# Kernel optimization log

Hardware: AMD Instinct MI355X
Metric: run time of the kernel (lower is better)

The kernel has to match this reference:

```python
import jax, jax.numpy as jnp
import numpy as np

D_MODEL = 1024
NUM_HEADS = 16
D_K = D_MODEL // NUM_HEADS
NEG_INF = -1e9


def setup_inputs() -> dict:
    key = jax.random.key(0)
    ks = jax.random.split(key, 12)
    B, S = 2, 2048
    scale = 1.0 / np.sqrt(D_MODEL)
    inp = {
        "q": jax.random.normal(ks[0], (B, S, D_MODEL), jnp.float32),
        "k": jax.random.normal(ks[1], (B, S, D_MODEL), jnp.float32),
        "v": jax.random.normal(ks[2], (B, S, D_MODEL), jnp.float32),
        "mask": jnp.ones((B, S), jnp.int32),
        "W_q": jax.random.normal(ks[3], (D_MODEL, D_MODEL), jnp.float32) * scale,
        "b_q": jnp.zeros((D_MODEL,), jnp.float32),
        "W_k": jax.random.normal(ks[4], (D_MODEL, D_MODEL), jnp.float32) * scale,
        "b_k": jnp.zeros((D_MODEL,), jnp.float32),
        "W_v": jax.random.normal(ks[5], (D_MODEL, D_MODEL), jnp.float32) * scale,
        "b_v": jnp.zeros((D_MODEL,), jnp.float32),
        "W_o": jax.random.normal(ks[6], (D_MODEL, D_MODEL), jnp.float32) * scale,
        "b_o": jnp.zeros((D_MODEL,), jnp.float32),
    }
    return inp


def reference(q, k, v, mask, W_q, b_q, W_k, b_k, W_v, b_v, W_o, b_o):
    B, S, _ = q.shape
    def proj(x, W, b):
        # [B,S,D] -> [B,H,S,d_k]
        y = x @ W.T + b
        return y.reshape(B, -1, NUM_HEADS, D_K).transpose(0, 2, 1, 3)
    qh = proj(q, W_q, b_q)
    kh = proj(k, W_k, b_k)
    vh = proj(v, W_v, b_v)
    scores = jnp.einsum("bhqd,bhkd->bhqk", qh, kh) / jnp.sqrt(jnp.float32(D_K))
    # 2D mask [B,S_k] -> broadcast over heads and query positions
    m = mask[:, None, None, :]
    scores = jnp.where(m == 0, jnp.float32(NEG_INF), scores)
    attn = jax.nn.softmax(scores, axis=-1)
    # dropout is identity at inference
    context = jnp.einsum("bhqk,bhkd->bhqd", attn, vh)
    context = context.transpose(0, 2, 1, 3).reshape(B, S, D_MODEL)
    return context @ W_o.T + b_o
```

## Files before the change

### kernel.cpp

```cpp
#include <hip/hip_runtime.h>
#include <hip/hip_bf16.h>
#include <cstdint>
#include <cstddef>

#define DMODEL 1024
#define NHEADS 16
#define DK 64
#define SEQ 2048
#define BATCH 2
#define NT (SEQ / 32)

typedef short bf16x8 __attribute__((ext_vector_type(8)));
typedef float f32x4 __attribute__((ext_vector_type(4)));
typedef float f32x16 __attribute__((ext_vector_type(16)));
typedef unsigned int u32x2 __attribute__((ext_vector_type(2)));
typedef unsigned int u32x4 __attribute__((ext_vector_type(4)));

typedef const __attribute__((address_space(1))) void* gas_ptr;
typedef __attribute__((address_space(3))) void* las_ptr;

__device__ __forceinline__ void gld_lds16(const void* g, void* l) {
    __builtin_amdgcn_global_load_lds((gas_ptr)g, (las_ptr)l, 16, 0, 0);
}

__device__ __forceinline__ ushort f2bf_u(float f) {
    uint32_t x = __float_as_uint(f);
    x += 0x7fff + ((x >> 16) & 1);
    return (ushort)(x >> 16);
}

__global__ __launch_bounds__(256) void cast_all(
        const float* __restrict__ q, const float* __restrict__ k,
        const float* __restrict__ v, const float* __restrict__ Wq,
        const float* __restrict__ Wk, const float* __restrict__ Wv,
        const float* __restrict__ Wo,
        ushort* __restrict__ qb, ushort* __restrict__ kb, ushort* __restrict__ vb,
        ushort* __restrict__ Wqb, ushort* __restrict__ Wkb,
        ushort* __restrict__ Wvb, ushort* __restrict__ Wob) {
    int bid = blockIdx.x;
    const float* src; ushort* dst; int base;
    if      (bid <  4096) { src = q;  dst = qb;  base = bid; }
    else if (bid <  8192) { src = k;  dst = kb;  base = bid - 4096; }
    else if (bid < 12288) { src = v;  dst = vb;  base = bid - 8192; }
    else if (bid < 13312) { src = Wq; dst = Wqb; base = bid - 12288; }
    else if (bid < 14336) { src = Wk; dst = Wkb; base = bid - 13312; }
    else if (bid < 15360) { src = Wv; dst = Wvb; base = bid - 14336; }
    else                  { src = Wo; dst = Wob; base = bid - 15360; }
    int i = base * 1024 + threadIdx.x * 4;
    float4 f = *reinterpret_cast<const float4*>(src + i);
    ushort4 o;
    o.x = f2bf_u(f.x); o.y = f2bf_u(f.y); o.z = f2bf_u(f.z); o.w = f2bf_u(f.w);
    *reinterpret_cast<ushort4*>(dst + i) = o;
}

__global__ __launch_bounds__(256) void mask2bias(
        const int* __restrict__ m, float* __restrict__ mb) {
    int i = (blockIdx.x * 256 + threadIdx.x) * 4;
    int4 mk = *reinterpret_cast<const int4*>(m + i);
    float4 o;
    o.x = mk.x ? 0.f : -1e9f;
    o.y = mk.y ? 0.f : -1e9f;
    o.z = mk.z ? 0.f : -1e9f;
    o.w = mk.w ? 0.f : -1e9f;
    *reinterpret_cast<float4*>(mb + i) = o;
}

template<int MODE>
__global__ __launch_bounds__(256) void gemm_bt(
        const ushort* __restrict__ A,
        const ushort* __restrict__ W,
        const float* __restrict__ bias,
        void* __restrict__ out, int M, int N, int K) {
    __shared__ ushort As[64 * 32];
    __shared__ ushort Bs[128 * 32];
    const int tid = threadIdx.x;
    const int w = tid >> 6, lane = tid & 63;
    const int lr = lane & 15, lg = lane >> 4;
    const int nTiles = N >> 7;
    const int nwg = gridDim.x;
    const int cpx = nwg >> 3;
    int lid = (blockIdx.x & 7) * cpx + (blockIdx.x >> 3);
    const int tM = (lid / nTiles) << 6;
    const int tN = (lid % nTiles) << 7;
    const int wr = (w >> 1) * 32, wc = (w & 1) * 64;

    f32x4 acc[2][4] = {};

    const int cA = w * 64 + lane;
    const int cB0 = w * 128 + lane;
    const int cB1 = w * 128 + 64 + lane;
    const ushort* gA  = A + (size_t)(tM + (cA  >> 2)) * K + (cA  & 3) * 8;
    const ushort* gB0 = W + (size_t)(tN + (cB0 >> 2)) * K + (cB0 & 3) * 8;
    const ushort* gB1 = W + (size_t)(tN + (cB1 >> 2)) * K + (cB1 & 3) * 8;
    ushort* lA  = As + w * 512;
    ushort* lB0 = Bs + w * 1024;
    ushort* lB1 = Bs + w * 1024 + 512;

    for (int k0 = 0; k0 < K; k0 += 32) {
        gld_lds16(gA  + k0, lA);
        gld_lds16(gB0 + k0, lB0);
        gld_lds16(gB1 + k0, lB1);
        __syncthreads();

        bf16x8 af[2], bfr[4];
#pragma unroll
        for (int i = 0; i < 2; i++)
            af[i] = *(const bf16x8*)(As + (wr + i * 16 + lr) * 32 + lg * 8);
#pragma unroll
        for (int i = 0; i < 4; i++)
            bfr[i] = *(const bf16x8*)(Bs + (wc + i * 16 + lr) * 32 + lg * 8);
#pragma unroll
        for (int mi = 0; mi < 2; mi++)
#pragma unroll
            for (int ni = 0; ni < 4; ni++)
                acc[mi][ni] = __builtin_amdgcn_mfma_f32_16x16x32_bf16(
                    af[mi], bfr[ni], acc[mi][ni], 0, 0, 0);
        __syncthreads();
    }

#pragma unroll
    for (int mi = 0; mi < 2; mi++) {
        const int row0 = tM + wr + mi * 16 + lg * 4;
#pragma unroll
        for (int ni = 0; ni < 4; ni++) {
            const int col = tN + wc + ni * 16 + lr;
            const float bv = bias[col];
#pragma unroll
            for (int r = 0; r < 4; r++) {
                float vv = acc[mi][ni][r] + bv;
                int m = row0 + r;
                if (MODE == 2) {
                    ((float*)out)[(size_t)m * N + col] = vv;
                } else {
                    int b = m >> 11, s = m & (SEQ - 1);
                    int h = col >> 6, d = col & (DK - 1);
                    if (MODE == 0)
                        ((ushort*)out)[(((size_t)(b * NHEADS + h) * SEQ + s) * DK) + d] = f2bf_u(vv);
                    else
                        ((ushort*)out)[(((size_t)(b * NHEADS + h) * DK + d) * SEQ) + s] = f2bf_u(vv);
                }
            }
        }
    }
}

#define SCALE2 0.18033688011120542f

__device__ __forceinline__ bf16x8 pack_pa(const float* p) {
    uint a, b, c, d;
    asm("v_cvt_pk_bf16_f32 %0, %1, %2" : "=v"(a) : "v"(p[0]), "v"(p[1]));
    asm("v_cvt_pk_bf16_f32 %0, %1, %2" : "=v"(b) : "v"(p[4]), "v"(p[5]));
    asm("v_cvt_pk_bf16_f32 %0, %1, %2" : "=v"(c) : "v"(p[2]), "v"(p[3]));
    asm("v_cvt_pk_bf16_f32 %0, %1, %2" : "=v"(d) : "v"(p[6]), "v"(p[7]));
    asm("v_permlane32_swap_b32 %0, %1" : "+v"(a), "+v"(b));
    asm("v_permlane32_swap_b32 %0, %1" : "+v"(c), "+v"(d));
    union { u32x4 u; bf16x8 h; } cv;
    cv.u = (u32x4){a, c, b, d};
    return cv.h;
}

__device__ __forceinline__ float xmax32(float x) {
    u32x2 r = __builtin_amdgcn_permlane32_swap(__float_as_uint(x), __float_as_uint(x), false, false);
    return fmaxf(__uint_as_float(r[0]), __uint_as_float(r[1]));
}
__device__ __forceinline__ float xadd32(float x) {
    u32x2 r = __builtin_amdgcn_permlane32_swap(__float_as_uint(x), __float_as_uint(x), false, false);
    return __uint_as_float(r[0]) + __uint_as_float(r[1]);
}

__global__ __launch_bounds__(256) void attn_fwd32(
        const ushort* __restrict__ Qh, const ushort* __restrict__ Kh,
        const ushort* __restrict__ Vt, const float* __restrict__ mbias,
        ushort* __restrict__ ctx) {
    __shared__ ushort Ks[2][2048];
    __shared__ ushort Vs[2][2048];
    __shared__ float  Ml[SEQ];

    const int tid = threadIdx.x;
    const int w = tid >> 6;
    const int l = tid & 63;
    const int q32 = l & 31, hi = l >> 5;
    const int q7 = q32 & 7;

    int lid = (blockIdx.x & 7) * 64 + (blockIdx.x >> 3);
    const int qblk = lid & 15;
    const int bh = lid >> 4;
    const int b = bh >> 4, h = bh & 15;
    const int q0 = qblk * 128 + w * 32;

    const ushort* Qp = Qh + (size_t)bh * SEQ * DK + (size_t)(q0 + q32) * DK + hi * 8;
    const ushort* Kg = Kh + (size_t)bh * SEQ * DK;
    const ushort* Vg = Vt + (size_t)bh * DK * SEQ;

    const int srow = tid >> 3;
    const int scs  = (tid & 7) ^ (srow & 7);
    const ushort* Ksrc = Kg + (size_t)srow * DK + scs * 8;
    const ushort* Vsrc = Vg + (size_t)(srow + ((scs & 4) << 3)) * SEQ + (scs & 3) * 8;

    {
        const float* mg = mbias + (size_t)b * SEQ;
        gld_lds16(mg + tid * 4,        &Ml[w * 256]);
        gld_lds16(mg + 1024 + tid * 4, &Ml[1024 + w * 256]);
    }

    auto STAGE = [&](int buf, int t) {
        const int kv0 = t * 32;
        gld_lds16(Ksrc + (size_t)kv0 * DK, &Ks[buf][w * 512]);
        gld_lds16(Vsrc + kv0,              &Vs[buf][w * 512]);
    };

    bf16x8 qf[4];
#pragma unroll
    for (int dc = 0; dc < 4; dc++)
        qf[dc] = *(const bf16x8*)(Qp + dc * 16);

    f32x16 c0 = {}, c1 = {};
    float m2 = -1e30f, lrun = 0.f;

    STAGE(0, 0);
    __syncthreads();

    for (int t = 0; t < NT; ++t) {
        const int buf = t & 1;
        if (t + 1 < NT) STAGE(buf ^ 1, t + 1);

        const ushort* Kb = &Ks[buf][0];
        const ushort* Vb = &Vs[buf][0];

        bf16x8 kf[4];
#pragma unroll
        for (int dc = 0; dc < 4; dc++)
            kf[dc] = *(const bf16x8*)(Kb + q32 * 64 + (((dc * 2 + hi) ^ q7) * 8));
        f32x16 s = {};
        __builtin_amdgcn_s_setprio(1);
#pragma unroll
        for (int dc = 0; dc < 4; dc++)
            s = __builtin_amdgcn_mfma_f32_32x32x16_bf16(kf[dc], qf[dc], s, 0, 0, 0);
        __builtin_amdgcn_s_setprio(0);

        const int kv0 = t * 32;
        float4 mb[4];
#pragma unroll
        for (int g = 0; g < 4; g++)
            mb[g] = *reinterpret_cast<const float4*>(&Ml[kv0 + g * 8 + hi * 4]);
        float p[16];
#pragma unroll
        for (int r = 0; r < 16; r++)
            p[r] = fmaf(s[r], SCALE2, reinterpret_cast<const float*>(&mb[r >> 2])[r & 3]);

        float m01 = fmaxf(p[0], p[1]),   m23 = fmaxf(p[2], p[3]);
        float m45 = fmaxf(p[4], p[5]),   m67 = fmaxf(p[6], p[7]);
        float m89 = fmaxf(p[8], p[9]),   mab = fmaxf(p[10], p[11]);
        float mcd = fmaxf(p[12], p[13]), mef = fmaxf(p[14], p[15]);
        float pm = fmaxf(fmaxf(fmaxf(m01, m23), fmaxf(m45, m67)),
                         fmaxf(fmaxf(m89, mab), fmaxf(mcd, mef)));
        pm = xmax32(pm);
        if (__any(pm - m2 > 8.0f)) {
            float mnew = fmaxf(m2, pm);
            float alpha = __builtin_amdgcn_exp2f(m2 - mnew);
            m2 = mnew; lrun *= alpha;
#pragma unroll
            for (int r = 0; r < 16; r++) {
                float aT = __shfl(alpha, (r & 3) + 8 * (r >> 2) + 4 * hi);
                c0[r] *= aT; c1[r] *= aT;
            }
        }

        float rs = 0.f;
#pragma unroll
        for (int r = 0; r < 16; r++) {
            p[r] = __builtin_amdgcn_exp2f(p[r] - m2);
            rs += p[r];
        }
        lrun += xadd32(rs);

        bf16x8 pa0 = pack_pa(p);
        bf16x8 pa1 = pack_pa(p + 8);

        bf16x8 vc[4];
#pragma unroll
        for (int dt = 0; dt < 2; dt++)
#pragma unroll
            for (int ks = 0; ks < 2; ks++)
                vc[dt * 2 + ks] = *(const bf16x8*)(Vb + q32 * 64 + (((dt * 4 + ks * 2 + hi) ^ q7) * 8));

        __builtin_amdgcn_s_setprio(1);
        c0 = __builtin_amdgcn_mfma_f32_32x32x16_bf16(pa0, vc[0], c0, 0, 0, 0);
        c1 = __builtin_amdgcn_mfma_f32_32x32x16_bf16(pa0, vc[2], c1, 0, 0, 0);
        c0 = __builtin_amdgcn_mfma_f32_32x32x16_bf16(pa1, vc[1], c0, 0, 0, 0);
        c1 = __builtin_amdgcn_mfma_f32_32x32x16_bf16(pa1, vc[3], c1, 0, 0, 0);
        __builtin_amdgcn_s_setprio(0);

        __syncthreads();
    }

    float rl = 1.0f / lrun;
#pragma unroll
    for (int r = 0; r < 16; r++) {
        int crow = (r & 3) + 8 * (r >> 2) + 4 * hi;
        float rlT = __shfl(rl, crow);
        int qq = q0 + crow;
        size_t base = (size_t)(b * SEQ + qq) * DMODEL + h * DK;
        ctx[base + q32]      = f2bf_u(c0[r] * rlT);
        ctx[base + 32 + q32] = f2bf_u(c1[r] * rlT);
    }
}

extern "C" void kernel_launch(void* const* d_in, const int* in_sizes, int n_in,
                              void* d_out, int out_size, void* d_ws, size_t ws_size,
                              hipStream_t stream) {
    const float* q    = (const float*)d_in[0];
    const float* k    = (const float*)d_in[1];
    const float* v    = (const float*)d_in[2];
    const int*   mask = (const int*)d_in[3];
    const float* Wq   = (const float*)d_in[4];
    const float* bq   = (const float*)d_in[5];
    const float* Wk   = (const float*)d_in[6];
    const float* bk   = (const float*)d_in[7];
    const float* Wv   = (const float*)d_in[8];
    const float* bv   = (const float*)d_in[9];
    const float* Wo   = (const float*)d_in[10];
    const float* bo   = (const float*)d_in[11];

    char* ws = (char*)d_ws;
    ushort* qb   = (ushort*)(ws + (size_t)0);
    ushort* kb   = (ushort*)(ws + ((size_t)8  << 20));
    ushort* vb   = (ushort*)(ws + ((size_t)16 << 20));
    ushort* Wqb  = (ushort*)(ws + ((size_t)24 << 20));
    ushort* Wkb  = (ushort*)(ws + ((size_t)26 << 20));
    ushort* Wvb  = (ushort*)(ws + ((size_t)28 << 20));
    ushort* Wob  = (ushort*)(ws + ((size_t)30 << 20));
    ushort* Qh   = (ushort*)(ws + ((size_t)32 << 20));
    ushort* Kh   = (ushort*)(ws + ((size_t)40 << 20));
    ushort* Vt   = (ushort*)(ws + ((size_t)48 << 20));
    ushort* ctxb = (ushort*)(ws + ((size_t)56 << 20));
    float*  mbias = (float*)(ws + (size_t)0);

    cast_all<<<16384, 256, 0, stream>>>(q, k, v, Wq, Wk, Wv, Wo,
                                        qb, kb, vb, Wqb, Wkb, Wvb, Wob);

    const int M = BATCH * SEQ;
    const int gemmGrid = (M / 64) * (DMODEL / 128);
    gemm_bt<0><<<gemmGrid, 256, 0, stream>>>(qb, Wqb, bq, Qh, M, DMODEL, DMODEL);
    gemm_bt<0><<<gemmGrid, 256, 0, stream>>>(kb, Wkb, bk, Kh, M, DMODEL, DMODEL);
    gemm_bt<1><<<gemmGrid, 256, 0, stream>>>(vb, Wvb, bv, Vt, M, DMODEL, DMODEL);

    mask2bias<<<BATCH * SEQ / 1024, 256, 0, stream>>>(mask, mbias);

    attn_fwd32<<<BATCH * NHEADS * (SEQ / 128), 256, 0, stream>>>(Qh, Kh, Vt, mbias, ctxb);

    gemm_bt<2><<<gemmGrid, 256, 0, stream>>>(ctxb, Wob, bo, (void*)d_out, M, DMODEL, DMODEL);
}
```

Before: 161.7 us.

## Double-buffer GEMM LDS and give each attention wave private register-staged K/V buffers

The projection GEMM gets double-buffered shared-memory tiles, so the next K-slice's global-to-LDS load is issued before the current slice's MFMAs. The attention kernel drops block-wide syncs by giving each wave its own K/V LDS copy, prefetched two tiles ahead through registers. The mask bias is now read straight from global memory instead of LDS. This trades four times the K/V global traffic per block and extra register pressure for fewer barriers. The GEMM loop still ends with a sync after compute, and the new loads are not waited on before that barrier, which raises a correctness question about the first buffer.

```diff
diff --git a/kernel.cpp b/kernel.cpp
--- a/kernel.cpp
+++ b/kernel.cpp
@@ -71,8 +71,8 @@
         const ushort* __restrict__ W,
         const float* __restrict__ bias,
         void* __restrict__ out, int M, int N, int K) {
-    __shared__ ushort As[64 * 32];
-    __shared__ ushort Bs[128 * 32];
+    __shared__ ushort As[2][64 * 32];
+    __shared__ ushort Bs[2][128 * 32];
     const int tid = threadIdx.x;
     const int w = tid >> 6, lane = tid & 63;
     const int lr = lane & 15, lg = lane >> 4;
@@ -92,23 +92,27 @@
     const ushort* gA  = A + (size_t)(tM + (cA  >> 2)) * K + (cA  & 3) * 8;
     const ushort* gB0 = W + (size_t)(tN + (cB0 >> 2)) * K + (cB0 & 3) * 8;
     const ushort* gB1 = W + (size_t)(tN + (cB1 >> 2)) * K + (cB1 & 3) * 8;
-    ushort* lA  = As + w * 512;
-    ushort* lB0 = Bs + w * 1024;
-    ushort* lB1 = Bs + w * 1024 + 512;
+
+    auto STAGE = [&](int buf, int k0) {
+        gld_lds16(gA  + k0, &As[buf][w * 512]);
+        gld_lds16(gB0 + k0, &Bs[buf][w * 1024]);
+        gld_lds16(gB1 + k0, &Bs[buf][w * 1024 + 512]);
+    };
+
+    STAGE(0, 0);
+    __syncthreads();
 
     for (int k0 = 0; k0 < K; k0 += 32) {
-        gld_lds16(gA  + k0, lA);
-        gld_lds16(gB0 + k0, lB0);
-        gld_lds16(gB1 + k0, lB1);
-        __syncthreads();
+        const int buf = (k0 >> 5) & 1;
+        if (k0 + 32 < K) STAGE(buf ^ 1, k0 + 32);
 
         bf16x8 af[2], bfr[4];
 #pragma unroll
         for (int i = 0; i < 2; i++)
-            af[i] = *(const bf16x8*)(As + (wr + i * 16 + lr) * 32 + lg * 8);
-#pragma unroll
-        for (int i = 0; i < 4; i++)
-            bfr[i] = *(const bf16x8*)(Bs + (wc + i * 16 + lr) * 32 + lg * 8);
+            af[i] = *(const bf16x8*)(&As[buf][(wr + i * 16 + lr) * 32 + lg * 8]);
+#pragma unroll
+        for (int i = 0; i < 4; i++)
+            bfr[i] = *(const bf16x8*)(&Bs[buf][(wc + i * 16 + lr) * 32 + lg * 8]);
 #pragma unroll
         for (int mi = 0; mi < 2; mi++)
 #pragma unroll
@@ -172,15 +176,14 @@
         const ushort* __restrict__ Qh, const ushort* __restrict__ Kh,
         const ushort* __restrict__ Vt, const float* __restrict__ mbias,
         ushort* __restrict__ ctx) {
-    __shared__ ushort Ks[2][2048];
-    __shared__ ushort Vs[2][2048];
-    __shared__ float  Ml[SEQ];
+    __shared__ ushort Ks[4][2][32 * 64];
+    __shared__ ushort Vs[4][2][32 * 64];
 
     const int tid = threadIdx.x;
     const int w = tid >> 6;
     const int l = tid & 63;
     const int q32 = l & 31, hi = l >> 5;
-    const int q7 = q32 & 7;
+    const int q7 = l & 7;
 
     int lid = (blockIdx.x & 7) * 64 + (blockIdx.x >> 3);
     const int qblk = lid & 15;
@@ -191,22 +194,31 @@
     const ushort* Qp = Qh + (size_t)bh * SEQ * DK + (size_t)(q0 + q32) * DK + hi * 8;
     const ushort* Kg = Kh + (size_t)bh * SEQ * DK;
     const ushort* Vg = Vt + (size_t)bh * DK * SEQ;
-
-    const int srow = tid >> 3;
-    const int scs  = (tid & 7) ^ (srow & 7);
-    const ushort* Ksrc = Kg + (size_t)srow * DK + scs * 8;
-    const ushort* Vsrc = Vg + (size_t)(srow + ((scs & 4) << 3)) * SEQ + (scs & 3) * 8;
-
-    {
-        const float* mg = mbias + (size_t)b * SEQ;
-        gld_lds16(mg + tid * 4,        &Ml[w * 256]);
-        gld_lds16(mg + 1024 + tid * 4, &Ml[1024 + w * 256]);
-    }
-
-    auto STAGE = [&](int buf, int t) {
+    const float* mrow = mbias + b * SEQ + hi * 4;
+
+    const int lg8 = l >> 3;
+    const int c8  = l & 7;
+    const int cs  = c8 ^ lg8;
+    const ushort* KsrcB = Kg + (size_t)lg8 * DK + cs * 8;
+    const ushort* VsrcB = Vg + (size_t)(lg8 + ((cs & 4) << 3)) * SEQ + (cs & 3) * 8;
+
+    bf16x8 kst[4], vst[4];
+    auto LOADSTAGE = [&](int t) {
         const int kv0 = t * 32;
-        gld_lds16(Ksrc + (size_t)kv0 * DK, &Ks[buf][w * 512]);
-        gld_lds16(Vsrc + kv0,              &Vs[buf][w * 512]);
+#pragma unroll
+        for (int i = 0; i < 4; i++)
+            kst[i] = *(const bf16x8*)(KsrcB + (size_t)(kv0 + i * 8) * DK);
+#pragma unroll
+        for (int i = 0; i < 4; i++)
+            vst[i] = *(const bf16x8*)(VsrcB + (size_t)i * 8 * SEQ + kv0);
+    };
+    auto WRITESTAGE = [&](int buf) {
+#pragma unroll
+        for (int i = 0; i < 4; i++)
+            *(bf16x8*)(&Ks[w][buf][(i * 8 + lg8) * 64 + c8 * 8]) = kst[i];
+#pragma unroll
+        for (int i = 0; i < 4; i++)
+            *(bf16x8*)(&Vs[w][buf][(i * 8 + lg8) * 64 + c8 * 8]) = vst[i];
     };
 
     bf16x8 qf[4];
@@ -217,20 +229,23 @@
     f32x16 c0 = {}, c1 = {};
     float m2 = -1e30f, lrun = 0.f;
 
-    STAGE(0, 0);
-    __syncthreads();
+    LOADSTAGE(0);
+    WRITESTAGE(0);
+    LOADSTAGE(1);
 
     for (int t = 0; t < NT; ++t) {
         const int buf = t & 1;
-        if (t + 1 < NT) STAGE(buf ^ 1, t + 1);
-
-        const ushort* Kb = &Ks[buf][0];
-        const ushort* Vb = &Vs[buf][0];
+        const int kv0 = t * 32;
+
+        float4 mb[4];
+#pragma unroll
+        for (int g = 0; g < 4; g++)
+            mb[g] = *reinterpret_cast<const float4*>(mrow + kv0 + g * 8);
 
         bf16x8 kf[4];
 #pragma unroll
         for (int dc = 0; dc < 4; dc++)
-            kf[dc] = *(const bf16x8*)(Kb + q32 * 64 + (((dc * 2 + hi) ^ q7) * 8));
+            kf[dc] = *(const bf16x8*)(&Ks[w][buf][q32 * 64 + (((dc * 2 + hi) ^ q7) * 8)]);
         f32x16 s = {};
         __builtin_amdgcn_s_setprio(1);
 #pragma unroll
@@ -238,11 +253,6 @@
             s = __builtin_amdgcn_mfma_f32_32x32x16_bf16(kf[dc], qf[dc], s, 0, 0, 0);
         __builtin_amdgcn_s_setprio(0);
 
-        const int kv0 = t * 32;
-        float4 mb[4];
-#pragma unroll
-        for (int g = 0; g < 4; g++)
-            mb[g] = *reinterpret_cast<const float4*>(&Ml[kv0 + g * 8 + hi * 4]);
         float p[16];
 #pragma unroll
         for (int r = 0; r < 16; r++)
@@ -282,7 +292,7 @@
         for (int dt = 0; dt < 2; dt++)
 #pragma unroll
             for (int ks = 0; ks < 2; ks++)
-                vc[dt * 2 + ks] = *(const bf16x8*)(Vb + q32 * 64 + (((dt * 4 + ks * 2 + hi) ^ q7) * 8));
+                vc[dt * 2 + ks] = *(const bf16x8*)(&Vs[w][buf][q32 * 64 + (((dt * 4 + ks * 2 + hi) ^ q7) * 8)]);
 
         __builtin_amdgcn_s_setprio(1);
         c0 = __builtin_amdgcn_mfma_f32_32x32x16_bf16(pa0, vc[0], c0, 0, 0, 0);
@@ -291,7 +301,8 @@
         c1 = __builtin_amdgcn_mfma_f32_32x32x16_bf16(pa1, vc[3], c1, 0, 0, 0);
         __builtin_amdgcn_s_setprio(0);
 
-        __syncthreads();
+        if (t + 1 < NT) WRITESTAGE(buf ^ 1);
+        if (t + 2 < NT) LOADSTAGE(t + 2);
     }
 
     float rl = 1.0f / lrun;
```

Measured after the change: 163.4 us. No clear change (+1.0%).

## Fuse Q/K/V projections into one batched GEMM launch with 128x128 tiles

Applied to the files above, without the earlier changes.

Replaces three separate projection GEMM launches with a single kernel that treats the q, k and v activations, which sit contiguously in the workspace, as a 3x-tall M dimension. Each block picks its weight matrix and bias by which third of M it covers, and writes to the Q, K or transposed V layout. Tiles grow from 64x128 to 128x128, with 4x4 MFMA accumulators per wave, to increase data reuse. This removes launch overhead and tail effects but doubles per-thread accumulator registers, which may lower occupancy.

```diff
diff --git a/kernel.cpp b/kernel.cpp
--- a/kernel.cpp
+++ b/kernel.cpp
@@ -65,20 +65,97 @@
     *reinterpret_cast<float4*>(mb + i) = o;
 }
 
-template<int MODE>
-__global__ __launch_bounds__(256) void gemm_bt(
+__global__ __launch_bounds__(256) void gemm_qkv(
+        const ushort* __restrict__ A,
+        const ushort* __restrict__ Wall,
+        const float* __restrict__ bq, const float* __restrict__ bk,
+        const float* __restrict__ bv,
+        ushort* __restrict__ Qh, ushort* __restrict__ Kh, ushort* __restrict__ Vt) {
+    __shared__ ushort As[128 * 32];
+    __shared__ ushort Bs[128 * 32];
+    const int tid = threadIdx.x;
+    const int w = tid >> 6, lane = tid & 63;
+    const int lr = lane & 15, lg = lane >> 4;
+    int lid = (blockIdx.x & 7) * 96 + (blockIdx.x >> 3);
+    const int tMg = (lid >> 3) << 7;
+    const int tN  = (lid & 7) << 7;
+    const int g   = tMg >> 12;
+    const ushort* W = Wall + (size_t)g * 1024 * 1024;
+    const float* bias = (g == 0) ? bq : (g == 1 ? bk : bv);
+    const int wr = (w >> 1) * 64, wc = (w & 1) * 64;
+
+    f32x4 acc[4][4] = {};
+
+    const int c0 = (w * 2 + 0) * 64 + lane;
+    const int c1 = (w * 2 + 1) * 64 + lane;
+    const ushort* gA0 = A + (size_t)(tMg + (c0 >> 2)) * 1024 + (c0 & 3) * 8;
+    const ushort* gA1 = A + (size_t)(tMg + (c1 >> 2)) * 1024 + (c1 & 3) * 8;
+    const ushort* gB0 = W + (size_t)(tN + (c0 >> 2)) * 1024 + (c0 & 3) * 8;
+    const ushort* gB1 = W + (size_t)(tN + (c1 >> 2)) * 1024 + (c1 & 3) * 8;
+    ushort* lA0 = As + (w * 2 + 0) * 512;
+    ushort* lA1 = As + (w * 2 + 1) * 512;
+    ushort* lB0 = Bs + (w * 2 + 0) * 512;
+    ushort* lB1 = Bs + (w * 2 + 1) * 512;
+
+    for (int k0 = 0; k0 < 1024; k0 += 32) {
+        gld_lds16(gA0 + k0, lA0);
+        gld_lds16(gA1 + k0, lA1);
+        gld_lds16(gB0 + k0, lB0);
+        gld_lds16(gB1 + k0, lB1);
+        __syncthreads();
+
+        bf16x8 af[4], bfr[4];
+#pragma unroll
+        for (int i = 0; i < 4; i++)
+            af[i] = *(const bf16x8*)(As + (wr + i * 16 + lr) * 32 + lg * 8);
+#pragma unroll
+        for (int i = 0; i < 4; i++)
+            bfr[i] = *(const bf16x8*)(Bs + (wc + i * 16 + lr) * 32 + lg * 8);
+#pragma unroll
+        for (int mi = 0; mi < 4; mi++)
+#pragma unroll
+            for (int ni = 0; ni < 4; ni++)
+                acc[mi][ni] = __builtin_amdgcn_mfma_f32_16x16x32_bf16(
+                    af[mi], bfr[ni], acc[mi][ni], 0, 0, 0);
+        __syncthreads();
+    }
+
+#pragma unroll
+    for (int mi = 0; mi < 4; mi++) {
+        const int row0 = tMg + wr + mi * 16 + lg * 4;
+#pragma unroll
+        for (int ni = 0; ni < 4; ni++) {
+            const int col = tN + wc + ni * 16 + lr;
+            const int h = col >> 6, d = col & (DK - 1);
+            const float bvv = bias[col];
+#pragma unroll
+            for (int r = 0; r < 4; r++) {
+                float vv = acc[mi][ni][r] + bvv;
+                int mloc = (row0 + r) & 4095;
+                int b = mloc >> 11, s = mloc & (SEQ - 1);
+                if (g == 0)
+                    Qh[(((size_t)(b * NHEADS + h) * SEQ + s) * DK) + d] = f2bf_u(vv);
+                else if (g == 1)
+                    Kh[(((size_t)(b * NHEADS + h) * SEQ + s) * DK) + d] = f2bf_u(vv);
+                else
+                    Vt[(((size_t)(b * NHEADS + h) * DK + d) * SEQ) + s] = f2bf_u(vv);
+            }
+        }
+    }
+}
+
+__global__ __launch_bounds__(256) void gemm_out(
         const ushort* __restrict__ A,
         const ushort* __restrict__ W,
         const float* __restrict__ bias,
-        void* __restrict__ out, int M, int N, int K) {
+        float* __restrict__ out, int M, int N, int K) {
     __shared__ ushort As[64 * 32];
     __shared__ ushort Bs[128 * 32];
     const int tid = threadIdx.x;
     const int w = tid >> 6, lane = tid & 63;
     const int lr = lane & 15, lg = lane >> 4;
     const int nTiles = N >> 7;
-    const int nwg = gridDim.x;
-    const int cpx = nwg >> 3;
+    const int cpx = gridDim.x >> 3;
     int lid = (blockIdx.x & 7) * cpx + (blockIdx.x >> 3);
     const int tM = (lid / nTiles) << 6;
     const int tN = (lid % nTiles) << 7;
@@ -126,20 +203,8 @@
             const int col = tN + wc + ni * 16 + lr;
             const float bv = bias[col];
 #pragma unroll
-            for (int r = 0; r < 4; r++) {
-                float vv = acc[mi][ni][r] + bv;
-                int m = row0 + r;
-                if (MODE == 2) {
-                    ((float*)out)[(size_t)m * N + col] = vv;
-                } else {
-                    int b = m >> 11, s = m & (SEQ - 1);
-                    int h = col >> 6, d = col & (DK - 1);
-                    if (MODE == 0)
-                        ((ushort*)out)[(((size_t)(b * NHEADS + h) * SEQ + s) * DK) + d] = f2bf_u(vv);
-                    else
-                        ((ushort*)out)[(((size_t)(b * NHEADS + h) * DK + d) * SEQ) + s] = f2bf_u(vv);
-                }
-            }
+            for (int r = 0; r < 4; r++)
+                out[(size_t)(row0 + r) * N + col] = acc[mi][ni][r] + bv;
         }
     }
 }
@@ -180,12 +245,13 @@
     const int w = tid >> 6;
     const int l = tid & 63;
     const int q32 = l & 31, hi = l >> 5;
-    const int q7 = q32 & 7;
+    const int q7 = l & 7;
 
     int lid = (blockIdx.x & 7) * 64 + (blockIdx.x >> 3);
     const int qblk = lid & 15;
     const int bh = lid >> 4;
-    const int b = bh >> 4, h = bh & 15;
+    const int b = bh >> 4;
+    const int h = bh & 15;
     const int q0 = qblk * 128 + w * 32;
 
     const ushort* Qp = Qh + (size_t)bh * SEQ * DK + (size_t)(q0 + q32) * DK + hi * 8;
@@ -339,15 +405,13 @@
     cast_all<<<16384, 256, 0, stream>>>(q, k, v, Wq, Wk, Wv, Wo,
                                         qb, kb, vb, Wqb, Wkb, Wvb, Wob);
 
+    gemm_qkv<<<768, 256, 0, stream>>>(qb, Wqb, bq, bk, bv, Qh, Kh, Vt);
+
+    mask2bias<<<BATCH * SEQ / 1024, 256, 0, stream>>>(mask, mbias);
+
+    attn_fwd32<<<BATCH * NHEADS * (SEQ / 128), 256, 0, stream>>>(Qh, Kh, Vt, mbias, ctxb);
+
     const int M = BATCH * SEQ;
-    const int gemmGrid = (M / 64) * (DMODEL / 128);
-    gemm_bt<0><<<gemmGrid, 256, 0, stream>>>(qb, Wqb, bq, Qh, M, DMODEL, DMODEL);
-    gemm_bt<0><<<gemmGrid, 256, 0, stream>>>(kb, Wkb, bk, Kh, M, DMODEL, DMODEL);
-    gemm_bt<1><<<gemmGrid, 256, 0, stream>>>(vb, Wvb, bv, Vt, M, DMODEL, DMODEL);
-
-    mask2bias<<<BATCH * SEQ / 1024, 256, 0, stream>>>(mask, mbias);
-
-    attn_fwd32<<<BATCH * NHEADS * (SEQ / 128), 256, 0, stream>>>(Qh, Kh, Vt, mbias, ctxb);
-
-    gemm_bt<2><<<gemmGrid, 256, 0, stream>>>(ctxb, Wob, bo, (void*)d_out, M, DMODEL, DMODEL);
-}
+    gemm_out<<<(M / 64) * (DMODEL / 128), 256, 0, stream>>>(
+        ctxb, Wob, bo, (float*)d_out, M, DMODEL, DMODEL);
+}
```

Result: faster. 152.1 us (-6.0%).
